# Optimization experiments

Measured on AMD Instinct MI355X. Metric: run time of the kernel, lower is better.

Reference implementation:

```python
import jax, jax.numpy as jnp
import numpy as np

EMB = 1024   # embedding_size = input_size // 2
HID = 1024   # hidden_size
B = 16384


def _glorot(key, shape):
    fan_in = shape[0]
    bound = 1.0 / np.sqrt(fan_in)
    return jax.random.uniform(key, shape, jnp.float32, -bound, bound)


def setup_inputs() -> dict:
    key = jax.random.key(0)
    ks = jax.random.split(key, 14)
    return {
        "inputs": jax.random.normal(ks[0], (B, 2 * EMB), jnp.float32),
        "state": jax.random.normal(ks[1], (B, HID), jnp.float32),
        # weights stored [in, out] (transpose of torch Linear layout)
        "Wr": _glorot(ks[2], (EMB + HID, HID)), "br": jnp.zeros((HID,), jnp.float32),
        "Wu": _glorot(ks[3], (EMB + HID, HID)), "bu": jnp.zeros((HID,), jnp.float32),
        "Wc": _glorot(ks[4], (EMB + HID, HID)), "bc": jnp.zeros((HID,), jnp.float32),
        "W1": _glorot(ks[5], (EMB, HID)), "b1": jnp.zeros((HID,), jnp.float32),
        "W2": _glorot(ks[6], (EMB, HID)), "b2": jnp.zeros((HID,), jnp.float32),
        "Wg": _glorot(ks[7], (2 * HID, HID)), "bg": jnp.zeros((HID,), jnp.float32),
    }


def reference(inputs, state, Wr, br, Wu, bu, Wc, bc, W1, b1, W2, b2, Wg, bg):
    # split input into semantic half and neighbor half
    x = inputs[:, :EMB]          # [B, EMB]
    neighbors = inputs[:, EMB:]  # [B, EMB]

    gate_inputs = jnp.concatenate([x, state], axis=1)            # [B, EMB+HID]
    r = jax.nn.sigmoid(gate_inputs @ Wr + br)                    # reset gate
    u = jax.nn.sigmoid(gate_inputs @ Wu + bu)                    # update gate
    c = jnp.tanh(jnp.concatenate([x, r * state], axis=1) @ Wc + bc)

    semantic_emb = jax.nn.relu(x @ W1 + b1)
    neighbor_emb = jax.nn.relu(neighbors @ W2 + b2)
    new_gate = jax.nn.sigmoid(
        jnp.concatenate([semantic_emb, neighbor_emb], axis=1) @ Wg + bg)

    new_h = u * state + (1.0 - u) * c * new_gate
    return new_h
```

## Files before the change

### kernel.cpp

```cpp
#include <hip/hip_runtime.h>
#include <hip/hip_bf16.h>
#include <math.h>

#define Bsz 16384
#define HIDc 1024

typedef __attribute__((ext_vector_type(8))) short short8_t;
typedef __attribute__((ext_vector_type(4))) float f32x4;
typedef __attribute__((ext_vector_type(4))) short s16x4;

typedef __attribute__((address_space(1))) const unsigned char* gp1_t;
typedef __attribute__((address_space(3))) unsigned char* lp3_t;

__device__ __forceinline__ float sigf(float x) { return 1.0f / (1.0f + __expf(-x)); }
__device__ __forceinline__ float tanh_fast(float x) {
  x = fminf(fmaxf(x, -10.f), 10.f);
  float t = __expf(2.f * x);
  return (t - 1.f) / (t + 1.f);
}

__device__ __forceinline__ int xcd_map(int bid, int nwg) {
  const int q = nwg >> 3, r = nwg & 7;
  const int xcd = bid & 7, idx = bid >> 3;
  return (xcd < r ? xcd * (q + 1) : r * (q + 1) + (xcd - r) * q) + idx;
}

__device__ __forceinline__ void stage_half(const __hip_bfloat16* __restrict__ g, long ld,
                                           __hip_bfloat16* l, int tid) {
#pragma unroll
  for (int it = 0; it < 2; ++it) {
    const int sid = it * 512 + tid;
    const int row = sid >> 3, slot = sid & 7;
    const int kx = (slot ^ (row & 7)) << 3;
    __builtin_amdgcn_global_load_lds((gp1_t)(g + (long)row * ld + kx),
                                     (lp3_t)(l + sid * 8), 16, 0, 0);
  }
}

#define STAGE_TILE(dstbase, t) do {                                              \
    stage_half(Ablk + (long)(t) * 64,             lda, (dstbase),         tid);  \
    stage_half(Ablk + 128 * lda + (long)(t) * 64, lda, (dstbase) + 8192,  tid);  \
    stage_half(Wblk + (long)(t) * 64,             ldw, (dstbase) + 16384, tid);  \
    stage_half(Wblk + 128 * ldw + (long)(t) * 64, ldw, (dstbase) + 24576, tid);  \
  } while (0)

#define READ_A(AhB, qm)                                                          \
  _Pragma("unroll") for (int m_ = 0; m_ < 4; ++m_)                               \
    _Pragma("unroll") for (int k_ = 0; k_ < 2; ++k_)                             \
      a8[m_][k_] = *reinterpret_cast<const short8_t*>(                           \
          (AhB) + ((qm) * 64 + m_ * 16 + lm) * 64 + (((k_ * 4 + hi) ^ l7) << 3));

#define READ_B(BhB, qn)                                                          \
  _Pragma("unroll") for (int n_ = 0; n_ < 2; ++n_)                               \
    _Pragma("unroll") for (int k_ = 0; k_ < 2; ++k_)                             \
      b8[qn][n_][k_] = *reinterpret_cast<const short8_t*>(                       \
          (BhB) + (wcl * 64 + (qn) * 32 + n_ * 16 + lm) * 64 + (((k_ * 4 + hi) ^ l7) << 3));

#define PHASE(qm, qn, VM) do {                                                   \
    __builtin_amdgcn_sched_barrier(0);                                           \
    __builtin_amdgcn_s_barrier();                                                \
    asm volatile("s_waitcnt lgkmcnt(0)" ::: "memory");                           \
    __builtin_amdgcn_sched_barrier(0);                                           \
    __builtin_amdgcn_s_setprio(1);                                               \
    _Pragma("unroll") for (int m_ = 0; m_ < 4; ++m_)                             \
      _Pragma("unroll") for (int n_ = 0; n_ < 2; ++n_)                           \
        _Pragma("unroll") for (int k_ = 0; k_ < 2; ++k_)                         \
          acc[qm][qn][m_][n_] = __builtin_amdgcn_mfma_f32_16x16x32_bf16(         \
              a8[m_][k_], b8[qn][n_][k_], acc[qm][qn][m_][n_], 0, 0, 0);         \
    __builtin_amdgcn_s_setprio(0);                                               \
    __builtin_amdgcn_sched_barrier(0);                                           \
    if (VM) {                                                                    \
      asm volatile("s_waitcnt vmcnt(0)" ::: "memory");                           \
      __builtin_amdgcn_sched_barrier(0);                                         \
    }                                                                            \
    __builtin_amdgcn_s_barrier();                                                \
    __builtin_amdgcn_sched_barrier(0);                                           \
  } while (0)

template <int EPI>
__global__ __launch_bounds__(512, 2)
void gemm256(const __hip_bfloat16* __restrict__ A, long lda,
             const __hip_bfloat16* __restrict__ Wt, long ldw, int K, int nbx,
             const float* __restrict__ bias0, const float* __restrict__ bias1,
             const __hip_bfloat16* __restrict__ stbf,
             const __hip_bfloat16* __restrict__ auxbf,
             const __hip_bfloat16* __restrict__ CB,
             const __hip_bfloat16* __restrict__ U,
             __hip_bfloat16* __restrict__ out0,
             __hip_bfloat16* __restrict__ out1,
             float* __restrict__ outf) {
  __shared__ __hip_bfloat16 lds[65536];
  const int tid = threadIdx.x;
  const int wave = tid >> 6, lane = tid & 63;
  const int wr = wave >> 2, wc = wave & 3, wcl = wc & 1;
  const int lm = lane & 15, hi = lane >> 4, l7 = lane & 7;

  const int wg = xcd_map(blockIdx.x, gridDim.x);
  const long mBase = (long)(wg / nbx) * 256;
  const long nBase = (long)(wg % nbx) * 256;
  const __hip_bfloat16* Ablk = A + mBase * lda;
  const __hip_bfloat16* Wblk = Wt + nBase * ldw;

  f32x4 acc[2][2][4][2];
#pragma unroll
  for (int a = 0; a < 2; ++a)
#pragma unroll
    for (int b = 0; b < 2; ++b)
#pragma unroll
      for (int c = 0; c < 4; ++c)
#pragma unroll
        for (int d = 0; d < 2; ++d) acc[a][b][c][d] = (f32x4){0.f, 0.f, 0.f, 0.f};

  short8_t a8[4][2], b8[2][2][2];

  STAGE_TILE(lds, 0);
  asm volatile("s_waitcnt vmcnt(0)" ::: "memory");
  __builtin_amdgcn_s_barrier();
  __builtin_amdgcn_sched_barrier(0);

  const int NI = K >> 7;
  for (int i = 0; i < NI; ++i) {
    {
      const __hip_bfloat16* AhB = lds + wr * 8192;
      const __hip_bfloat16* BhB = lds + 16384 + (wc >> 1) * 8192;
      READ_A(AhB, 0); READ_B(BhB, 0);
      STAGE_TILE(lds + 32768, 2 * i + 1);
      PHASE(0, 0, 0);
      READ_B(BhB, 1);
      PHASE(0, 1, 0);
      READ_A(AhB, 1);
      PHASE(1, 0, 0);
      PHASE(1, 1, 1);
    }
    {
      const __hip_bfloat16* AhB = lds + 32768 + wr * 8192;
      const __hip_bfloat16* BhB = lds + 32768 + 16384 + (wc >> 1) * 8192;
      READ_A(AhB, 0); READ_B(BhB, 0);
      if (i + 1 < NI) STAGE_TILE(lds, 2 * i + 2);
      PHASE(0, 0, 0);
      READ_B(BhB, 1);
      PHASE(0, 1, 0);
      READ_A(AhB, 1);
      PHASE(1, 0, 0);
      PHASE(1, 1, 1);
    }
  }

#pragma unroll
  for (int qm = 0; qm < 2; ++qm)
#pragma unroll
    for (int qn = 0; qn < 2; ++qn)
#pragma unroll
      for (int m = 0; m < 4; ++m)
#pragma unroll
        for (int n = 0; n < 2; ++n)
#pragma unroll
          for (int j = 0; j < 4; ++j) {
            const long row = mBase + wr * 128 + qm * 64 + m * 16 + hi * 4 + j;
            const int col = (int)nBase + wc * 64 + qn * 32 + n * 16 + lm;
            const float v = acc[qm][qn][m][n][j];
            if (EPI == 0) {
              if (col < HIDc) {
                float rr = sigf(v + bias0[col]);
                float st = __bfloat162float(stbf[row * 2048 + 1024 + col]);
                out0[row * HIDc + col] = __float2bfloat16(rr * st);
              } else {
                int c = col - HIDc;
                out1[row * HIDc + c] = __float2bfloat16(sigf(v + bias1[c]));
              }
            } else if (EPI == 1) {
              if (col < HIDc) {
                out0[row * 2048 + col] = __float2bfloat16(fmaxf(v + bias0[col], 0.f));
              } else {
                int c = col - HIDc;
                out1[row * HIDc + c] = __float2bfloat16(v + bias1[c]);
              }
            } else if (EPI == 2) {
              out0[row * 2048 + HIDc + col] = __float2bfloat16(fmaxf(v + bias0[col], 0.f));
            } else if (EPI == 3) {
              const long idx = row * HIDc + col;
              out0[idx] = __float2bfloat16(tanh_fast(v + __bfloat162float(auxbf[idx])));
            } else {
              const long idx = row * HIDc + col;
              float g = sigf(v + bias0[col]);
              float u = __bfloat162float(U[idx]);
              float cb = __bfloat162float(CB[idx]);
              float st = __bfloat162float(stbf[row * 2048 + 1024 + col]);
              outf[idx] = u * st + (1.f - u) * cb * g;
            }
          }
}

__global__ void convert_k(const float4* __restrict__ in4, const float4* __restrict__ st4,
                          __hip_bfloat16* __restrict__ A1, __hip_bfloat16* __restrict__ NB) {
  const long NI4 = (long)Bsz * 2048 / 4;
  const long NS4 = (long)Bsz * 1024 / 4;
  for (long i = (long)blockIdx.x * blockDim.x + threadIdx.x; i < NI4 + NS4;
       i += (long)gridDim.x * blockDim.x) {
    float4 v;
    __hip_bfloat16* dst;
    if (i < NI4) {
      v = in4[i];
      long e = i << 2;
      long row = e >> 11;
      int col = (int)(e & 2047);
      dst = (col < 1024) ? (A1 + row * 2048 + col) : (NB + row * 1024 + (col - 1024));
    } else {
      long j = i - NI4;
      v = st4[j];
      long e = j << 2;
      long row = e >> 10;
      int col = (int)(e & 1023);
      dst = A1 + row * 2048 + 1024 + col;
    }
    union { __hip_bfloat16 h[4]; s16x4 s; } u;
    u.h[0] = __float2bfloat16(v.x);
    u.h[1] = __float2bfloat16(v.y);
    u.h[2] = __float2bfloat16(v.z);
    u.h[3] = __float2bfloat16(v.w);
    *reinterpret_cast<s16x4*>(dst) = u.s;
  }
}

__global__ void transpose_k(const float* __restrict__ in, int ldin,
                            __hip_bfloat16* __restrict__ out, long ldout) {
  __shared__ float t[32][33];
  const int k0 = blockIdx.x * 32, n0 = blockIdx.y * 32;
  const int tx = threadIdx.x, ty = threadIdx.y;
#pragma unroll
  for (int dy = 0; dy < 32; dy += 8)
    t[ty + dy][tx] = in[(long)(k0 + ty + dy) * ldin + n0 + tx];
  __syncthreads();
#pragma unroll
  for (int dy = 0; dy < 32; dy += 8)
    out[(long)(n0 + ty + dy) * ldout + k0 + tx] = __float2bfloat16(t[tx][ty + dy]);
}

extern "C" void kernel_launch(void* const* d_in, const int* in_sizes, int n_in,
                              void* d_out, int out_size, void* d_ws, size_t ws_size,
                              hipStream_t stream) {
  const float* inputs = (const float*)d_in[0];
  const float* state = (const float*)d_in[1];
  const float* Wr = (const float*)d_in[2];
  const float* br = (const float*)d_in[3];
  const float* Wu = (const float*)d_in[4];
  const float* bu = (const float*)d_in[5];
  const float* Wc = (const float*)d_in[6];
  const float* bc = (const float*)d_in[7];
  const float* W1 = (const float*)d_in[8];
  const float* b1 = (const float*)d_in[9];
  const float* W2 = (const float*)d_in[10];
  const float* b2 = (const float*)d_in[11];
  const float* Wg = (const float*)d_in[12];
  const float* bg = (const float*)d_in[13];
  float* out = (float*)d_out;

  char* ws = (char*)d_ws;
  __hip_bfloat16* A1    = (__hip_bfloat16*)(ws);
  __hip_bfloat16* NB    = (__hip_bfloat16*)(ws + 67108864L);
  __hip_bfloat16* RS    = (__hip_bfloat16*)(ws + 100663296L);
  __hip_bfloat16* Ub    = (__hip_bfloat16*)(ws + 134217728L);
  __hip_bfloat16* SN    = (__hip_bfloat16*)(ws + 167772160L);
  __hip_bfloat16* CXb   = (__hip_bfloat16*)(ws + 234881024L);
  __hip_bfloat16* Wru_t = (__hip_bfloat16*)(ws + 268435456L);
  __hip_bfloat16* W1cx_t= (__hip_bfloat16*)(ws + 276824064L);
  __hip_bfloat16* Wcb_t = (__hip_bfloat16*)(ws + 281018368L);
  __hip_bfloat16* W2_t  = (__hip_bfloat16*)(ws + 283115520L);
  __hip_bfloat16* Wg_t  = (__hip_bfloat16*)(ws + 285212672L);
  __hip_bfloat16* CB    = NB;

  convert_k<<<2048, 256, 0, stream>>>((const float4*)inputs, (const float4*)state, A1, NB);

  dim3 tb(32, 8);
  transpose_k<<<dim3(64, 32), tb, 0, stream>>>(Wr, 1024, Wru_t, 2048);
  transpose_k<<<dim3(64, 32), tb, 0, stream>>>(Wu, 1024, Wru_t + (long)1024 * 2048, 2048);
  transpose_k<<<dim3(32, 32), tb, 0, stream>>>(W1, 1024, W1cx_t, 1024);
  transpose_k<<<dim3(32, 32), tb, 0, stream>>>(Wc, 1024, W1cx_t + (long)1024 * 1024, 1024);
  transpose_k<<<dim3(32, 32), tb, 0, stream>>>(Wc + (long)1024 * 1024, 1024, Wcb_t, 1024);
  transpose_k<<<dim3(32, 32), tb, 0, stream>>>(W2, 1024, W2_t, 1024);
  transpose_k<<<dim3(64, 32), tb, 0, stream>>>(Wg, 1024, Wg_t, 2048);

  gemm256<0><<<512, 512, 0, stream>>>(A1, 2048, Wru_t, 2048, 2048, 8,
                                      br, bu, A1, nullptr, nullptr, nullptr,
                                      RS, Ub, nullptr);
  gemm256<1><<<512, 512, 0, stream>>>(A1, 2048, W1cx_t, 1024, 1024, 8,
                                      b1, bc, nullptr, nullptr, nullptr, nullptr,
                                      SN, CXb, nullptr);
  gemm256<2><<<256, 512, 0, stream>>>(NB, 1024, W2_t, 1024, 1024, 4,
                                      b2, nullptr, nullptr, nullptr, nullptr, nullptr,
                                      SN, nullptr, nullptr);
  gemm256<3><<<256, 512, 0, stream>>>(RS, 1024, Wcb_t, 1024, 1024, 4,
                                      nullptr, nullptr, nullptr, CXb, nullptr, nullptr,
                                      CB, nullptr, nullptr);
  gemm256<4><<<256, 512, 0, stream>>>(SN, 2048, Wg_t, 2048, 2048, 4,
                                      bg, nullptr, A1, nullptr, CB, Ub,
                                      nullptr, nullptr, out);
}
```

Baseline: 584.1 us.

## Restructure GEMM to 256x128 tiles with a three-stage LDS pipeline

```diff
diff --git a/kernel.cpp b/kernel.cpp
--- a/kernel.cpp
+++ b/kernel.cpp
@@ -25,62 +25,24 @@
   return (xcd < r ? xcd * (q + 1) : r * (q + 1) + (xcd - r) * q) + idx;
 }
 
-__device__ __forceinline__ void stage_half(const __hip_bfloat16* __restrict__ g, long ld,
-                                           __hip_bfloat16* l, int tid) {
-#pragma unroll
-  for (int it = 0; it < 2; ++it) {
-    const int sid = it * 512 + tid;
-    const int row = sid >> 3, slot = sid & 7;
-    const int kx = (slot ^ (row & 7)) << 3;
-    __builtin_amdgcn_global_load_lds((gp1_t)(g + (long)row * ld + kx),
-                                     (lp3_t)(l + sid * 8), 16, 0, 0);
-  }
-}
-
-#define STAGE_TILE(dstbase, t) do {                                              \
-    stage_half(Ablk + (long)(t) * 64,             lda, (dstbase),         tid);  \
-    stage_half(Ablk + 128 * lda + (long)(t) * 64, lda, (dstbase) + 8192,  tid);  \
-    stage_half(Wblk + (long)(t) * 64,             ldw, (dstbase) + 16384, tid);  \
-    stage_half(Wblk + 128 * ldw + (long)(t) * 64, ldw, (dstbase) + 24576, tid);  \
-  } while (0)
-
-#define READ_A(AhB, qm)                                                          \
-  _Pragma("unroll") for (int m_ = 0; m_ < 4; ++m_)                               \
-    _Pragma("unroll") for (int k_ = 0; k_ < 2; ++k_)                             \
-      a8[m_][k_] = *reinterpret_cast<const short8_t*>(                           \
-          (AhB) + ((qm) * 64 + m_ * 16 + lm) * 64 + (((k_ * 4 + hi) ^ l7) << 3));
-
-#define READ_B(BhB, qn)                                                          \
-  _Pragma("unroll") for (int n_ = 0; n_ < 2; ++n_)                               \
-    _Pragma("unroll") for (int k_ = 0; k_ < 2; ++k_)                             \
-      b8[qn][n_][k_] = *reinterpret_cast<const short8_t*>(                       \
-          (BhB) + (wcl * 64 + (qn) * 32 + n_ * 16 + lm) * 64 + (((k_ * 4 + hi) ^ l7) << 3));
-
-#define PHASE(qm, qn, VM) do {                                                   \
-    __builtin_amdgcn_sched_barrier(0);                                           \
-    __builtin_amdgcn_s_barrier();                                                \
-    asm volatile("s_waitcnt lgkmcnt(0)" ::: "memory");                           \
-    __builtin_amdgcn_sched_barrier(0);                                           \
-    __builtin_amdgcn_s_setprio(1);                                               \
-    _Pragma("unroll") for (int m_ = 0; m_ < 4; ++m_)                             \
-      _Pragma("unroll") for (int n_ = 0; n_ < 2; ++n_)                           \
-        _Pragma("unroll") for (int k_ = 0; k_ < 2; ++k_)                         \
-          acc[qm][qn][m_][n_] = __builtin_amdgcn_mfma_f32_16x16x32_bf16(         \
-              a8[m_][k_], b8[qn][n_][k_], acc[qm][qn][m_][n_], 0, 0, 0);         \
-    __builtin_amdgcn_s_setprio(0);                                               \
-    __builtin_amdgcn_sched_barrier(0);                                           \
-    if (VM) {                                                                    \
-      asm volatile("s_waitcnt vmcnt(0)" ::: "memory");                           \
-      __builtin_amdgcn_sched_barrier(0);                                         \
-    }                                                                            \
-    __builtin_amdgcn_s_barrier();                                                \
-    __builtin_amdgcn_sched_barrier(0);                                           \
+#define DSR(dst, addr, IMM) \
+  asm volatile("ds_read_b128 %0, %1 offset:" IMM : "=v"(dst) : "v"(addr))
+
+#define STAGE_ADV(BIDX) do {                                                                   \
+    __hip_bfloat16* db_ = lds + (BIDX) * 24576;                                                \
+    __builtin_amdgcn_global_load_lds((gp1_t)pa0, (lp3_t)(db_ + tid * 8), 16, 0, 0);            \
+    __builtin_amdgcn_global_load_lds((gp1_t)pa1, (lp3_t)(db_ + (512 + tid) * 8), 16, 0, 0);    \
+    __builtin_amdgcn_global_load_lds((gp1_t)pa2, (lp3_t)(db_ + (1024 + tid) * 8), 16, 0, 0);   \
+    __builtin_amdgcn_global_load_lds((gp1_t)pa3, (lp3_t)(db_ + (1536 + tid) * 8), 16, 0, 0);   \
+    __builtin_amdgcn_global_load_lds((gp1_t)pb0, (lp3_t)(db_ + 16384 + tid * 8), 16, 0, 0);    \
+    __builtin_amdgcn_global_load_lds((gp1_t)pb1, (lp3_t)(db_ + 16384 + (512 + tid) * 8), 16, 0, 0); \
+    pa0 += 64; pa1 += 64; pa2 += 64; pa3 += 64; pb0 += 64; pb1 += 64;                          \
   } while (0)
 
 template <int EPI>
 __global__ __launch_bounds__(512, 2)
 void gemm256(const __hip_bfloat16* __restrict__ A, long lda,
-             const __hip_bfloat16* __restrict__ Wt, long ldw, int K, int nbx,
+             const __hip_bfloat16* __restrict__ Wt, long ldw, int nbx,
              const float* __restrict__ bias0, const float* __restrict__ bias1,
              const __hip_bfloat16* __restrict__ stbf,
              const __hip_bfloat16* __restrict__ auxbf,
@@ -89,106 +51,116 @@
              __hip_bfloat16* __restrict__ out0,
              __hip_bfloat16* __restrict__ out1,
              float* __restrict__ outf) {
-  __shared__ __hip_bfloat16 lds[65536];
+  constexpr int KC = (EPI == 0 || EPI == 4) ? 2048 : 1024;
+  constexpr int NS = KC / 64;
+  __shared__ __hip_bfloat16 lds[3 * 24576];
+
   const int tid = threadIdx.x;
   const int wave = tid >> 6, lane = tid & 63;
-  const int wr = wave >> 2, wc = wave & 3, wcl = wc & 1;
+  const int wr = wave >> 1, wc = wave & 1;
   const int lm = lane & 15, hi = lane >> 4, l7 = lane & 7;
 
   const int wg = xcd_map(blockIdx.x, gridDim.x);
   const long mBase = (long)(wg / nbx) * 256;
-  const long nBase = (long)(wg % nbx) * 256;
+  const long nBase = (long)(wg % nbx) * 128;
   const __hip_bfloat16* Ablk = A + mBase * lda;
   const __hip_bfloat16* Wblk = Wt + nBase * ldw;
 
-  f32x4 acc[2][2][4][2];
-#pragma unroll
-  for (int a = 0; a < 2; ++a)
-#pragma unroll
-    for (int b = 0; b < 2; ++b)
-#pragma unroll
-      for (int c = 0; c < 4; ++c)
-#pragma unroll
-        for (int d = 0; d < 2; ++d) acc[a][b][c][d] = (f32x4){0.f, 0.f, 0.f, 0.f};
-
-  short8_t a8[4][2], b8[2][2][2];
-
-  STAGE_TILE(lds, 0);
-  asm volatile("s_waitcnt vmcnt(0)" ::: "memory");
-  __builtin_amdgcn_s_barrier();
-  __builtin_amdgcn_sched_barrier(0);
-
-  const int NI = K >> 7;
-  for (int i = 0; i < NI; ++i) {
-    {
-      const __hip_bfloat16* AhB = lds + wr * 8192;
-      const __hip_bfloat16* BhB = lds + 16384 + (wc >> 1) * 8192;
-      READ_A(AhB, 0); READ_B(BhB, 0);
-      STAGE_TILE(lds + 32768, 2 * i + 1);
-      PHASE(0, 0, 0);
-      READ_B(BhB, 1);
-      PHASE(0, 1, 0);
-      READ_A(AhB, 1);
-      PHASE(1, 0, 0);
-      PHASE(1, 1, 1);
-    }
-    {
-      const __hip_bfloat16* AhB = lds + 32768 + wr * 8192;
-      const __hip_bfloat16* BhB = lds + 32768 + 16384 + (wc >> 1) * 8192;
-      READ_A(AhB, 0); READ_B(BhB, 0);
-      if (i + 1 < NI) STAGE_TILE(lds, 2 * i + 2);
-      PHASE(0, 0, 0);
-      READ_B(BhB, 1);
-      PHASE(0, 1, 0);
-      READ_A(AhB, 1);
-      PHASE(1, 0, 0);
-      PHASE(1, 1, 1);
-    }
+  const int sidA[4] = {tid, 512 + tid, 1024 + tid, 1536 + tid};
+  const __hip_bfloat16 *pa0, *pa1, *pa2, *pa3, *pb0, *pb1;
+  {
+    int r0 = sidA[0] >> 3, r1 = sidA[1] >> 3, r2 = sidA[2] >> 3, r3 = sidA[3] >> 3;
+    pa0 = Ablk + (long)r0 * lda + (((sidA[0] & 7) ^ (r0 & 7)) << 3);
+    pa1 = Ablk + (long)r1 * lda + (((sidA[1] & 7) ^ (r1 & 7)) << 3);
+    pa2 = Ablk + (long)r2 * lda + (((sidA[2] & 7) ^ (r2 & 7)) << 3);
+    pa3 = Ablk + (long)r3 * lda + (((sidA[3] & 7) ^ (r3 & 7)) << 3);
+    pb0 = Wblk + (long)r0 * ldw + (((sidA[0] & 7) ^ (r0 & 7)) << 3);
+    pb1 = Wblk + (long)r1 * ldw + (((sidA[1] & 7) ^ (r1 & 7)) << 3);
   }
 
-#pragma unroll
-  for (int qm = 0; qm < 2; ++qm)
-#pragma unroll
-    for (int qn = 0; qn < 2; ++qn)
-#pragma unroll
-      for (int m = 0; m < 4; ++m)
-#pragma unroll
-        for (int n = 0; n < 2; ++n)
-#pragma unroll
-          for (int j = 0; j < 4; ++j) {
-            const long row = mBase + wr * 128 + qm * 64 + m * 16 + hi * 4 + j;
-            const int col = (int)nBase + wc * 64 + qn * 32 + n * 16 + lm;
-            const float v = acc[qm][qn][m][n][j];
-            if (EPI == 0) {
-              if (col < HIDc) {
-                float rr = sigf(v + bias0[col]);
-                float st = __bfloat162float(stbf[row * 2048 + 1024 + col]);
-                out0[row * HIDc + col] = __float2bfloat16(rr * st);
-              } else {
-                int c = col - HIDc;
-                out1[row * HIDc + c] = __float2bfloat16(sigf(v + bias1[c]));
-              }
-            } else if (EPI == 1) {
-              if (col < HIDc) {
-                out0[row * 2048 + col] = __float2bfloat16(fmaxf(v + bias0[col], 0.f));
-              } else {
-                int c = col - HIDc;
-                out1[row * HIDc + c] = __float2bfloat16(v + bias1[c]);
-              }
-            } else if (EPI == 2) {
-              out0[row * 2048 + HIDc + col] = __float2bfloat16(fmaxf(v + bias0[col], 0.f));
-            } else if (EPI == 3) {
-              const long idx = row * HIDc + col;
-              out0[idx] = __float2bfloat16(tanh_fast(v + __bfloat162float(auxbf[idx])));
-            } else {
-              const long idx = row * HIDc + col;
-              float g = sigf(v + bias0[col]);
-              float u = __bfloat162float(U[idx]);
-              float cb = __bfloat162float(CB[idx]);
-              float st = __bfloat162float(stbf[row * 2048 + 1024 + col]);
-              outf[idx] = u * st + (1.f - u) * cb * g;
-            }
+  const unsigned ldsbase = (unsigned)(size_t)(void*)lds;
+  const unsigned laneA = (unsigned)((wr * 64 + lm) * 128 + ((hi ^ l7) << 4));
+  const unsigned laneB = (unsigned)((wc * 64 + lm) * 128 + ((hi ^ l7) << 4));
+
+  f32x4 acc[4][4];
+#pragma unroll
+  for (int m = 0; m < 4; ++m)
+#pragma unroll
+    for (int n = 0; n < 4; ++n) acc[m][n] = (f32x4){0.f, 0.f, 0.f, 0.f};
+
+  STAGE_ADV(0);
+  STAGE_ADV(1);
+
+  for (int s = 0; s < NS; ++s) {
+    if (s == NS - 1) asm volatile("s_waitcnt vmcnt(0)" ::: "memory");
+    else             asm volatile("s_waitcnt vmcnt(6)" ::: "memory");
+    __builtin_amdgcn_s_barrier();
+
+    const unsigned base = ldsbase + (unsigned)((s % 3) * 49152);
+    unsigned a0 = base + laneA;
+    unsigned b0 = base + 32768u + laneB;
+    unsigned a1 = a0 ^ 64u, b1 = b0 ^ 64u;
+    short8_t a8[4][2], b8[4][2];
+    DSR(a8[0][0], a0, "0"); DSR(a8[1][0], a0, "2048"); DSR(a8[2][0], a0, "4096"); DSR(a8[3][0], a0, "6144");
+    DSR(a8[0][1], a1, "0"); DSR(a8[1][1], a1, "2048"); DSR(a8[2][1], a1, "4096"); DSR(a8[3][1], a1, "6144");
+    DSR(b8[0][0], b0, "0"); DSR(b8[1][0], b0, "2048"); DSR(b8[2][0], b0, "4096"); DSR(b8[3][0], b0, "6144");
+    DSR(b8[0][1], b1, "0"); DSR(b8[1][1], b1, "2048"); DSR(b8[2][1], b1, "4096"); DSR(b8[3][1], b1, "6144");
+
+    if (s + 2 < NS) STAGE_ADV((s + 2) % 3);
+
+    asm volatile("s_waitcnt lgkmcnt(0)" ::: "memory");
+    __builtin_amdgcn_sched_barrier(0);
+    __builtin_amdgcn_s_setprio(1);
+#pragma unroll
+    for (int ks = 0; ks < 2; ++ks)
+#pragma unroll
+      for (int mf = 0; mf < 4; ++mf)
+#pragma unroll
+        for (int nf = 0; nf < 4; ++nf)
+          acc[mf][nf] = __builtin_amdgcn_mfma_f32_16x16x32_bf16(a8[mf][ks], b8[nf][ks],
+                                                                acc[mf][nf], 0, 0, 0);
+    __builtin_amdgcn_s_setprio(0);
+  }
+
+#pragma unroll
+  for (int mf = 0; mf < 4; ++mf)
+#pragma unroll
+    for (int nf = 0; nf < 4; ++nf)
+#pragma unroll
+      for (int j = 0; j < 4; ++j) {
+        const long row = mBase + wr * 64 + mf * 16 + hi * 4 + j;
+        const int col = (int)nBase + wc * 64 + nf * 16 + lm;
+        const float v = acc[mf][nf][j];
+        if (EPI == 0) {
+          if (col < HIDc) {
+            float rr = sigf(v + bias0[col]);
+            float st = __bfloat162float(stbf[row * 2048 + 1024 + col]);
+            out0[row * HIDc + col] = __float2bfloat16(rr * st);
+          } else {
+            int c = col - HIDc;
+            out1[row * HIDc + c] = __float2bfloat16(sigf(v + bias1[c]));
           }
+        } else if (EPI == 1) {
+          if (col < HIDc) {
+            out0[row * 2048 + col] = __float2bfloat16(fmaxf(v + bias0[col], 0.f));
+          } else {
+            int c = col - HIDc;
+            out1[row * HIDc + c] = __float2bfloat16(v + bias1[c]);
+          }
+        } else if (EPI == 2) {
+          out0[row * 2048 + HIDc + col] = __float2bfloat16(fmaxf(v + bias0[col], 0.f));
+        } else if (EPI == 3) {
+          const long idx = row * HIDc + col;
+          out0[idx] = __float2bfloat16(tanh_fast(v + __bfloat162float(auxbf[idx])));
+        } else {
+          const long idx = row * HIDc + col;
+          float g = sigf(v + bias0[col]);
+          float u = __bfloat162float(U[idx]);
+          float cb = __bfloat162float(CB[idx]);
+          float st = __bfloat162float(stbf[row * 2048 + 1024 + col]);
+          outf[idx] = u * st + (1.f - u) * cb * g;
+        }
+      }
 }
 
 __global__ void convert_k(const float4* __restrict__ in4, const float4* __restrict__ st4,
@@ -280,19 +252,19 @@
   transpose_k<<<dim3(32, 32), tb, 0, stream>>>(W2, 1024, W2_t, 1024);
   transpose_k<<<dim3(64, 32), tb, 0, stream>>>(Wg, 1024, Wg_t, 2048);
 
-  gemm256<0><<<512, 512, 0, stream>>>(A1, 2048, Wru_t, 2048, 2048, 8,
-                                      br, bu, A1, nullptr, nullptr, nullptr,
-                                      RS, Ub, nullptr);
-  gemm256<1><<<512, 512, 0, stream>>>(A1, 2048, W1cx_t, 1024, 1024, 8,
-                                      b1, bc, nullptr, nullptr, nullptr, nullptr,
-                                      SN, CXb, nullptr);
-  gemm256<2><<<256, 512, 0, stream>>>(NB, 1024, W2_t, 1024, 1024, 4,
+  gemm256<0><<<1024, 512, 0, stream>>>(A1, 2048, Wru_t, 2048, 16,
+                                       br, bu, A1, nullptr, nullptr, nullptr,
+                                       RS, Ub, nullptr);
+  gemm256<1><<<1024, 512, 0, stream>>>(A1, 2048, W1cx_t, 1024, 16,
+                                       b1, bc, nullptr, nullptr, nullptr, nullptr,
+                                       SN, CXb, nullptr);
+  gemm256<2><<<512, 512, 0, stream>>>(NB, 1024, W2_t, 1024, 8,
                                       b2, nullptr, nullptr, nullptr, nullptr, nullptr,
                                       SN, nullptr, nullptr);
-  gemm256<3><<<256, 512, 0, stream>>>(RS, 1024, Wcb_t, 1024, 1024, 4,
+  gemm256<3><<<512, 512, 0, stream>>>(RS, 1024, Wcb_t, 1024, 8,
                                       nullptr, nullptr, nullptr, CXb, nullptr, nullptr,
                                       CB, nullptr, nullptr);
-  gemm256<4><<<256, 512, 0, stream>>>(SN, 2048, Wg_t, 2048, 2048, 4,
+  gemm256<4><<<512, 512, 0, stream>>>(SN, 2048, Wg_t, 2048, 8,
                                       bg, nullptr, A1, nullptr, CB, Ub,
                                       nullptr, nullptr, out);
 }
```

Measured after the change: 570.5 us. 1.02x faster.
